# Optimization experiments

Hardware: AMD Instinct MI355X
Metric: run time of the kernel (lower is better)

## Reference

```python
import jax, jax.numpy as jnp
import numpy as np

T, H, I = 32768, 2048, 768  # tokens, hidden_size, moe_intermediate_size


def setup_inputs() -> dict:
    key = jax.random.key(0)
    k1, k2, k3 = jax.random.split(key, 3)
    hidden_states = jax.random.normal(k1, (T, H), dtype=jnp.float32)
    # merged gate_up weight: columns [0:I] = gate, [I:2I] = up
    w_gate_up = jax.random.normal(k2, (H, 2 * I), dtype=jnp.float32) * 0.02
    w_down = jax.random.normal(k3, (I, H), dtype=jnp.float32) * 0.02
    return {"hidden_states": hidden_states, "w_gate_up": w_gate_up, "w_down": w_down}


def reference(hidden_states, w_gate_up, w_down):
    # gate_up projection: [T, H] @ [H, 2I] -> [T, 2I]
    gate_up = jnp.einsum('th,hf->tf', hidden_states, w_gate_up)
    gate, up = jnp.split(gate_up, 2, axis=-1)
    # SiluAndMul: silu(gate) * up -> [T, I]
    x = jax.nn.silu(gate) * up
    # down projection: [T, I] @ [I, H] -> [T, H]
    return jnp.einsum('ti,ih->th', x, w_down)
```

## Files before the change

kernel.cpp:

```cpp
#include <hip/hip_runtime.h>

#define T_TOK 32768
#define H_DIM 2048
#define I_DIM 768
#define N1_DIM 1536

typedef unsigned short ushort_t;
typedef __attribute__((ext_vector_type(8))) short  short8;
typedef __attribute__((ext_vector_type(4))) float  floatx4;

__device__ __forceinline__ ushort_t f2bf(float f) {
    union { float f; unsigned u; } v; v.f = f;
    unsigned u = v.u;
    unsigned r = (u + 0x7fffu + ((u >> 16) & 1u)) >> 16;
    return (ushort_t)r;
}
__device__ __forceinline__ float bf2f(ushort_t h) {
    union { unsigned u; float f; } v; v.u = ((unsigned)h) << 16;
    return v.f;
}

typedef __attribute__((address_space(1))) const void gq_t;
typedef __attribute__((address_space(3))) void lq_t;
__device__ __forceinline__ void gld_lds16(const void* g, void* l) {
    __builtin_amdgcn_global_load_lds((gq_t*)g, (lq_t*)l, 16, 0, 0);
}

__global__ __launch_bounds__(256) void cast_f32_bf16_k(
    const float* __restrict__ in, ushort_t* __restrict__ out)
{
    size_t i = ((size_t)blockIdx.x * 256 + threadIdx.x) * 8;
    const float4 a = *(const float4*)(in + i);
    const float4 b = *(const float4*)(in + i + 4);
    short8 o;
    o[0] = (short)f2bf(a.x); o[1] = (short)f2bf(a.y);
    o[2] = (short)f2bf(a.z); o[3] = (short)f2bf(a.w);
    o[4] = (short)f2bf(b.x); o[5] = (short)f2bf(b.y);
    o[6] = (short)f2bf(b.z); o[7] = (short)f2bf(b.w);
    *(short8*)(out + i) = o;
}

__global__ __launch_bounds__(256) void transpose_cast_k(
    const float* __restrict__ in, ushort_t* __restrict__ out, int R, int C)
{
    __shared__ float tile[32][33];
    const int c0 = blockIdx.x * 32;
    const int r0 = blockIdx.y * 32;
    const int tx = threadIdx.x;
    const int ty = threadIdx.y;
#pragma unroll
    for (int dy = 0; dy < 32; dy += 8)
        tile[ty + dy][tx] = in[(size_t)(r0 + ty + dy) * C + (c0 + tx)];
    __syncthreads();
#pragma unroll
    for (int dy = 0; dy < 32; dy += 8)
        out[(size_t)(c0 + ty + dy) * R + (r0 + tx)] = f2bf(tile[tx][ty + dy]);
}

template <bool BF16_OUT>
__global__ __launch_bounds__(256) void gemm_bt(
    const ushort_t* __restrict__ A, int lda,
    const ushort_t* __restrict__ Bt, int ldb,
    void* __restrict__ Cv, int ldc, int K)
{
    __shared__ ushort_t Asm[128 * 64];
    __shared__ ushort_t Bsm[128 * 64];

    const int tid  = threadIdx.x;
    const int lane = tid & 63;
    const int wave = tid >> 6;
    const int m0   = blockIdx.x * 128;
    const int n0   = blockIdx.y * 128;
    const int wm   = (wave >> 1) * 64;
    const int wn   = (wave & 1) * 64;
    const int s    = lane & 15;
    const int q    = lane >> 4;
    const int s7   = s & 7;

    const int srow = lane >> 3;
    const int skof = ((lane & 7) ^ srow) * 8;

    floatx4 acc[4][4];
#pragma unroll
    for (int i = 0; i < 4; ++i)
#pragma unroll
        for (int j = 0; j < 4; ++j)
            acc[i][j] = floatx4{0.f, 0.f, 0.f, 0.f};

    for (int kt = 0; kt < K; kt += 64) {
#pragma unroll
        for (int c = 0; c < 4; ++c) {
            const int ca = wave + c * 4;
            gld_lds16(A  + (size_t)(m0 + ca * 8 + srow) * lda + kt + skof, &Asm[ca * 512]);
            gld_lds16(Bt + (size_t)(n0 + ca * 8 + srow) * ldb + kt + skof, &Bsm[ca * 512]);
        }
        __syncthreads();
#pragma unroll
        for (int ks = 0; ks < 2; ++ks) {
            const int slot = ((ks * 4 + q) ^ s7) * 8;
            short8 av[4], bv[4];
#pragma unroll
            for (int i = 0; i < 4; ++i) {
                av[i] = *(const short8*)&Asm[(wm + i * 16 + s) * 64 + slot];
                bv[i] = *(const short8*)&Bsm[(wn + i * 16 + s) * 64 + slot];
            }
#pragma unroll
            for (int i = 0; i < 4; ++i)
#pragma unroll
                for (int j = 0; j < 4; ++j)
                    acc[i][j] = __builtin_amdgcn_mfma_f32_16x16x32_bf16(
                        av[i], bv[j], acc[i][j], 0, 0, 0);
        }
        __syncthreads();
    }

    const int cr = q * 4;
#pragma unroll
    for (int i = 0; i < 4; ++i) {
#pragma unroll
        for (int j = 0; j < 4; ++j) {
            const int r  = m0 + wm + i * 16 + cr;
            const int cn = n0 + wn + j * 16 + s;
#pragma unroll
            for (int t = 0; t < 4; ++t) {
                const float v = acc[i][j][t];
                if (BF16_OUT)
                    ((ushort_t*)Cv)[(size_t)(r + t) * ldc + cn] = f2bf(v);
                else
                    ((float*)Cv)[(size_t)(r + t) * ldc + cn] = v;
            }
        }
    }
}

__global__ __launch_bounds__(256) void silu_mul_k(
    const ushort_t* __restrict__ gu, ushort_t* __restrict__ x)
{
    const int idx = blockIdx.x * 256 + threadIdx.x;
    const int t   = idx / 96;
    const int c8  = (idx - t * 96) * 8;
    const short8 gv = *(const short8*)(gu + (size_t)t * N1_DIM + c8);
    const short8 uv = *(const short8*)(gu + (size_t)t * N1_DIM + I_DIM + c8);
    short8 xv;
#pragma unroll
    for (int e = 0; e < 8; ++e) {
        const float g = bf2f((ushort_t)gv[e]);
        const float u = bf2f((ushort_t)uv[e]);
        const float s = g / (1.0f + __expf(-g));
        xv[e] = (short)f2bf(s * u);
    }
    *(short8*)(x + (size_t)t * I_DIM + c8) = xv;
}

extern "C" void kernel_launch(void* const* d_in, const int* in_sizes, int n_in,
                              void* d_out, int out_size, void* d_ws, size_t ws_size,
                              hipStream_t stream)
{
    const float* hs  = (const float*)d_in[0];
    const float* wgu = (const float*)d_in[1];
    const float* wd  = (const float*)d_in[2];
    float*       out = (float*)d_out;

    char* ws = (char*)d_ws;
    ushort_t* wgu_t = (ushort_t*)ws;
    ushort_t* wd_t  = (ushort_t*)(ws + 6291456);
    ushort_t* xb    = (ushort_t*)(ws + 9437184);

    char* ob = (char*)d_out;
    ushort_t* gu_s = (ushort_t*)ob;
    ushort_t* hs_b = (ushort_t*)(ob + 100663296);

    cast_f32_bf16_k<<<32768, 256, 0, stream>>>(hs, hs_b);
    transpose_cast_k<<<dim3(N1_DIM / 32, H_DIM / 32), dim3(32, 8), 0, stream>>>(
        wgu, wgu_t, H_DIM, N1_DIM);
    transpose_cast_k<<<dim3(H_DIM / 32, I_DIM / 32), dim3(32, 8), 0, stream>>>(
        wd, wd_t, I_DIM, H_DIM);
    gemm_bt<true><<<dim3(T_TOK / 128, N1_DIM / 128), 256, 0, stream>>>(
        hs_b, H_DIM, wgu_t, H_DIM, (void*)gu_s, N1_DIM, H_DIM);
    silu_mul_k<<<(T_TOK * (I_DIM / 8)) / 256, 256, 0, stream>>>(gu_s, xb);
    gemm_bt<false><<<dim3(T_TOK / 128, H_DIM / 128), 256, 0, stream>>>(
        xb, I_DIM, wd_t, I_DIM, (void*)out, H_DIM, I_DIM);
}
```

Measured before the change: 890.7 us.

## Replace GEMMs with 256x256 pipelined kernel and fuse SiLU-mul into epilogue

Replaces the 128x128 single-buffered GEMM with a 512-thread 256x256-tile kernel that double-buffers LDS through direct global-to-LDS loads. It interleaves MFMA with the next tile's loads and uses setprio and explicit waitcnt and barriers. The gate/up weight rows are permuted in 16-column chunks so each wave holds matching gate and up columns, letting the first GEMM apply SiLU*up in its epilogue. This removes the bf16 gate_up round trip and the separate elementwise kernel. Block index swizzling aims to improve L2 reuse, at the cost of larger register pressure and 128KB LDS per block, which risks occupancy.

```diff
diff --git a/kernel.cpp b/kernel.cpp
--- a/kernel.cpp
+++ b/kernel.cpp
@@ -14,10 +14,6 @@
     unsigned u = v.u;
     unsigned r = (u + 0x7fffu + ((u >> 16) & 1u)) >> 16;
     return (ushort_t)r;
-}
-__device__ __forceinline__ float bf2f(ushort_t h) {
-    union { unsigned u; float f; } v; v.u = ((unsigned)h) << 16;
-    return v.f;
 }
 
 typedef __attribute__((address_space(1))) const void gq_t;
@@ -40,6 +36,13 @@
     *(short8*)(out + i) = o;
 }
 
+__device__ __forceinline__ int gu_perm(int c) {
+    const int t  = (c >= I_DIM) ? 1 : 0;
+    const int cc = c - t * I_DIM;
+    return ((cc >> 4) << 5) + (t << 4) + (cc & 15);
+}
+
+template <bool PERM>
 __global__ __launch_bounds__(256) void transpose_cast_k(
     const float* __restrict__ in, ushort_t* __restrict__ out, int R, int C)
 {
@@ -53,103 +56,167 @@
         tile[ty + dy][tx] = in[(size_t)(r0 + ty + dy) * C + (c0 + tx)];
     __syncthreads();
 #pragma unroll
-    for (int dy = 0; dy < 32; dy += 8)
-        out[(size_t)(c0 + ty + dy) * R + (r0 + tx)] = f2bf(tile[tx][ty + dy]);
-}
-
-template <bool BF16_OUT>
-__global__ __launch_bounds__(256) void gemm_bt(
-    const ushort_t* __restrict__ A, int lda,
-    const ushort_t* __restrict__ Bt, int ldb,
-    void* __restrict__ Cv, int ldc, int K)
-{
-    __shared__ ushort_t Asm[128 * 64];
-    __shared__ ushort_t Bsm[128 * 64];
+    for (int dy = 0; dy < 32; dy += 8) {
+        const int c = c0 + ty + dy;
+        const int orow = PERM ? gu_perm(c) : c;
+        out[(size_t)orow * R + (r0 + tx)] = f2bf(tile[tx][ty + dy]);
+    }
+}
+
+#define GB    __builtin_amdgcn_s_barrier()
+#define SB0   __builtin_amdgcn_sched_barrier(0)
+#define LGKM0 asm volatile("s_waitcnt lgkmcnt(0)" ::: "memory")
+#define VMW(N) asm volatile("s_waitcnt vmcnt(" #N ")" ::: "memory")
+
+template <int EPI>
+__global__ __launch_bounds__(512, 2) void gemm_bt8(
+    const ushort_t* __restrict__ A,
+    const ushort_t* __restrict__ Bt,
+    void* __restrict__ Cv,
+    int lda, int ldb, int ldc, int K)
+{
+    __shared__ __align__(16) ushort_t lds[65536];
 
     const int tid  = threadIdx.x;
     const int lane = tid & 63;
     const int wave = tid >> 6;
-    const int m0   = blockIdx.x * 128;
-    const int n0   = blockIdx.y * 128;
-    const int wm   = (wave >> 1) * 64;
-    const int wn   = (wave & 1) * 64;
+    const int wm   = (wave >> 2) * 128;
+    const int wn   = (wave & 3) * 64;
     const int s    = lane & 15;
     const int q    = lane >> 4;
-    const int s7   = s & 7;
-
-    const int srow = lane >> 3;
-    const int skof = ((lane & 7) ^ srow) * 8;
-
-    floatx4 acc[4][4];
-#pragma unroll
-    for (int i = 0; i < 4; ++i)
+
+    const int nwg = gridDim.x;
+    const int cpx = nwg >> 3;
+    const int wg  = blockIdx.x;
+    const int swz = (wg & 7) * cpx + (wg >> 3);
+    const int m0  = (swz & 127) * 256;
+    const int n0  = (swz >> 7) * 256;
+
+    const int srow = wave * 16 + (lane >> 2);
+    const int scol = (lane & 3) * 8;
+    const ushort_t* Ab = A  + (size_t)(m0 + srow) * lda + scol;
+    const ushort_t* Bb = Bt + (size_t)(n0 + srow) * ldb + scol;
+    ushort_t* ldsA = &lds[wave * 512];
+    ushort_t* ldsB = &lds[32768 + wave * 512];
+
+#define STAGE_A(kt, h, c, b) gld_lds16(Ab + (size_t)((c)*128) * lda + (kt) + (h)*32, \
+                                       ldsA + ((b)*2 + (h)) * 8192 + (c)*4096)
+#define STAGE_B(kt, h, c, b) gld_lds16(Bb + (size_t)((c)*128) * ldb + (kt) + (h)*32, \
+                                       ldsB + ((b)*2 + (h)) * 8192 + (c)*4096)
+
+    const int arow = wm + s;
+    const int brow = wn + s;
+#define LDA4(b, ks, mh, av) { _Pragma("unroll") for (int ii = 0; ii < 4; ++ii) \
+    av[ii] = *(const short8*)&lds[((b)*2 + (ks)) * 8192 + (arow + (mh)*64 + ii*16) * 32 + q*8]; }
+#define LDB4(b, ks, bv) { _Pragma("unroll") for (int jj = 0; jj < 4; ++jj) \
+    bv[jj] = *(const short8*)&lds[32768 + ((b)*2 + (ks)) * 8192 + (brow + jj*16) * 32 + q*8]; }
+#define MFMA16(mh, av, bv) { _Pragma("unroll") for (int ii = 0; ii < 4; ++ii) \
+    _Pragma("unroll") for (int jj = 0; jj < 4; ++jj) \
+        acc[(mh)*4 + ii][jj] = __builtin_amdgcn_mfma_f32_16x16x32_bf16( \
+            av[ii], bv[jj], acc[(mh)*4 + ii][jj], 0, 0, 0); }
+
+    floatx4 acc[8][4];
+#pragma unroll
+    for (int i = 0; i < 8; ++i)
 #pragma unroll
         for (int j = 0; j < 4; ++j)
             acc[i][j] = floatx4{0.f, 0.f, 0.f, 0.f};
 
-    for (int kt = 0; kt < K; kt += 64) {
-#pragma unroll
-        for (int c = 0; c < 4; ++c) {
-            const int ca = wave + c * 4;
-            gld_lds16(A  + (size_t)(m0 + ca * 8 + srow) * lda + kt + skof, &Asm[ca * 512]);
-            gld_lds16(Bt + (size_t)(n0 + ca * 8 + srow) * ldb + kt + skof, &Bsm[ca * 512]);
-        }
-        __syncthreads();
-#pragma unroll
-        for (int ks = 0; ks < 2; ++ks) {
-            const int slot = ((ks * 4 + q) ^ s7) * 8;
-            short8 av[4], bv[4];
-#pragma unroll
-            for (int i = 0; i < 4; ++i) {
-                av[i] = *(const short8*)&Asm[(wm + i * 16 + s) * 64 + slot];
-                bv[i] = *(const short8*)&Bsm[(wn + i * 16 + s) * 64 + slot];
-            }
-#pragma unroll
-            for (int i = 0; i < 4; ++i)
-#pragma unroll
-                for (int j = 0; j < 4; ++j)
-                    acc[i][j] = __builtin_amdgcn_mfma_f32_16x16x32_bf16(
-                        av[i], bv[j], acc[i][j], 0, 0, 0);
-        }
-        __syncthreads();
-    }
-
-    const int cr = q * 4;
-#pragma unroll
-    for (int i = 0; i < 4; ++i) {
-#pragma unroll
-        for (int j = 0; j < 4; ++j) {
-            const int r  = m0 + wm + i * 16 + cr;
-            const int cn = n0 + wn + j * 16 + s;
-#pragma unroll
-            for (int t = 0; t < 4; ++t) {
-                const float v = acc[i][j][t];
-                if (BF16_OUT)
-                    ((ushort_t*)Cv)[(size_t)(r + t) * ldc + cn] = f2bf(v);
-                else
-                    ((float*)Cv)[(size_t)(r + t) * ldc + cn] = v;
+    const int NT = K >> 6;
+
+    STAGE_A(0, 0, 0, 0); STAGE_A(0, 0, 1, 0);
+    STAGE_B(0, 0, 0, 0); STAGE_B(0, 0, 1, 0);
+    STAGE_A(0, 1, 0, 0); STAGE_A(0, 1, 1, 0);
+    STAGE_B(0, 1, 0, 0); STAGE_B(0, 1, 1, 0);
+    VMW(4);
+    GB; SB0;
+
+    for (int t = 0; t < NT - 1; ++t) {
+        const int b   = t & 1;
+        const int nb  = b ^ 1;
+        const int kt1 = (t + 1) << 6;
+        short8 av[4], bv[4];
+        LDA4(b, 0, 0, av); LDB4(b, 0, bv);
+        STAGE_A(kt1, 0, 0, nb); STAGE_A(kt1, 0, 1, nb);
+        GB; LGKM0; SB0;
+        __builtin_amdgcn_s_setprio(1); MFMA16(0, av, bv); __builtin_amdgcn_s_setprio(0);
+        GB;
+        LDA4(b, 0, 1, av);
+        STAGE_B(kt1, 0, 0, nb); STAGE_B(kt1, 0, 1, nb);
+        GB; LGKM0; SB0;
+        __builtin_amdgcn_s_setprio(1); MFMA16(1, av, bv); __builtin_amdgcn_s_setprio(0);
+        VMW(4);
+        GB;
+        LDA4(b, 1, 0, av); LDB4(b, 1, bv);
+        STAGE_A(kt1, 1, 0, nb); STAGE_A(kt1, 1, 1, nb);
+        GB; LGKM0; SB0;
+        __builtin_amdgcn_s_setprio(1); MFMA16(0, av, bv); __builtin_amdgcn_s_setprio(0);
+        GB;
+        LDA4(b, 1, 1, av);
+        STAGE_B(kt1, 1, 0, nb); STAGE_B(kt1, 1, 1, nb);
+        GB; LGKM0; SB0;
+        __builtin_amdgcn_s_setprio(1); MFMA16(1, av, bv); __builtin_amdgcn_s_setprio(0);
+        VMW(4);
+        GB;
+    }
+    {
+        const int b = (NT - 1) & 1;
+        short8 av[4], bv[4];
+        LDA4(b, 0, 0, av); LDB4(b, 0, bv);
+        GB; LGKM0; SB0;
+        __builtin_amdgcn_s_setprio(1); MFMA16(0, av, bv); __builtin_amdgcn_s_setprio(0);
+        GB;
+        LDA4(b, 0, 1, av);
+        GB; LGKM0; SB0;
+        __builtin_amdgcn_s_setprio(1); MFMA16(1, av, bv); __builtin_amdgcn_s_setprio(0);
+        VMW(0);
+        GB;
+        LDA4(b, 1, 0, av); LDB4(b, 1, bv);
+        GB; LGKM0; SB0;
+        __builtin_amdgcn_s_setprio(1); MFMA16(0, av, bv); __builtin_amdgcn_s_setprio(0);
+        GB;
+        LDA4(b, 1, 1, av);
+        LGKM0; SB0;
+        __builtin_amdgcn_s_setprio(1); MFMA16(1, av, bv); __builtin_amdgcn_s_setprio(0);
+    }
+
+    if (EPI == 0) {
+        float* C = (float*)Cv;
+#pragma unroll
+        for (int i = 0; i < 8; ++i) {
+            const int r = m0 + wm + i * 16 + q * 4;
+#pragma unroll
+            for (int j = 0; j < 4; ++j) {
+                const int cn = n0 + wn + j * 16 + s;
+#pragma unroll
+                for (int tt = 0; tt < 4; ++tt)
+                    C[(size_t)(r + tt) * ldc + cn] = acc[i][j][tt];
             }
         }
-    }
-}
-
-__global__ __launch_bounds__(256) void silu_mul_k(
-    const ushort_t* __restrict__ gu, ushort_t* __restrict__ x)
-{
-    const int idx = blockIdx.x * 256 + threadIdx.x;
-    const int t   = idx / 96;
-    const int c8  = (idx - t * 96) * 8;
-    const short8 gv = *(const short8*)(gu + (size_t)t * N1_DIM + c8);
-    const short8 uv = *(const short8*)(gu + (size_t)t * N1_DIM + I_DIM + c8);
-    short8 xv;
-#pragma unroll
-    for (int e = 0; e < 8; ++e) {
-        const float g = bf2f((ushort_t)gv[e]);
-        const float u = bf2f((ushort_t)uv[e]);
-        const float s = g / (1.0f + __expf(-g));
-        xv[e] = (short)f2bf(s * u);
-    }
-    *(short8*)(x + (size_t)t * I_DIM + c8) = xv;
+    } else {
+        ushort_t* X = (ushort_t*)Cv;
+        const int cb2 = (n0 + wn) >> 1;
+#pragma unroll
+        for (int i = 0; i < 8; ++i) {
+            const int r = m0 + wm + i * 16 + q * 4;
+#pragma unroll
+            for (int jp = 0; jp < 2; ++jp) {
+                const int cn = cb2 + jp * 16 + s;
+#pragma unroll
+                for (int tt = 0; tt < 4; ++tt) {
+                    const float g  = acc[i][2 * jp][tt];
+                    const float u  = acc[i][2 * jp + 1][tt];
+                    const float sv = g / (1.0f + __expf(-g));
+                    X[(size_t)(r + tt) * ldc + cn] = f2bf(sv * u);
+                }
+            }
+        }
+    }
+#undef STAGE_A
+#undef STAGE_B
+#undef LDA4
+#undef LDB4
+#undef MFMA16
 }
 
 extern "C" void kernel_launch(void* const* d_in, const int* in_sizes, int n_in,
@@ -166,18 +233,15 @@
     ushort_t* wd_t  = (ushort_t*)(ws + 6291456);
     ushort_t* xb    = (ushort_t*)(ws + 9437184);
 
-    char* ob = (char*)d_out;
-    ushort_t* gu_s = (ushort_t*)ob;
-    ushort_t* hs_b = (ushort_t*)(ob + 100663296);
+    ushort_t* hs_b = (ushort_t*)d_out;
 
     cast_f32_bf16_k<<<32768, 256, 0, stream>>>(hs, hs_b);
-    transpose_cast_k<<<dim3(N1_DIM / 32, H_DIM / 32), dim3(32, 8), 0, stream>>>(
+    transpose_cast_k<true><<<dim3(N1_DIM / 32, H_DIM / 32), dim3(32, 8), 0, stream>>>(
         wgu, wgu_t, H_DIM, N1_DIM);
-    transpose_cast_k<<<dim3(H_DIM / 32, I_DIM / 32), dim3(32, 8), 0, stream>>>(
+    transpose_cast_k<false><<<dim3(H_DIM / 32, I_DIM / 32), dim3(32, 8), 0, stream>>>(
         wd, wd_t, I_DIM, H_DIM);
-    gemm_bt<true><<<dim3(T_TOK / 128, N1_DIM / 128), 256, 0, stream>>>(
-        hs_b, H_DIM, wgu_t, H_DIM, (void*)gu_s, N1_DIM, H_DIM);
-    silu_mul_k<<<(T_TOK * (I_DIM / 8)) / 256, 256, 0, stream>>>(gu_s, xb);
-    gemm_bt<false><<<dim3(T_TOK / 128, H_DIM / 128), 256, 0, stream>>>(
-        xb, I_DIM, wd_t, I_DIM, (void*)out, H_DIM, I_DIM);
-}
+    gemm_bt8<1><<<(T_TOK / 256) * (N1_DIM / 256), 512, 0, stream>>>(
+        hs_b, wgu_t, (void*)xb, H_DIM, H_DIM, I_DIM, H_DIM);
+    gemm_bt8<0><<<(T_TOK / 256) * (H_DIM / 256), 512, 0, stream>>>(
+        xb, wd_t, (void*)out, I_DIM, I_DIM, H_DIM, I_DIM);
+}
```

Result: faster. 748.3 us (-16.0%).
